# Kernel optimization log

Hardware: AMD Instinct MI355X
Metric: run time of the kernel (lower is better)

Reference implementation:

```python
import jax, jax.numpy as jnp
import numpy as np

KERNEL_D = 3          # cv2 d=3 -> radius 1, 3x3 neighborhood
SIGMA_SPACE = 50.0
SIGMA_COLOR = 2.0
POOL = 16             # downsample_factor


def _bilateral3(x):
    # x: [B, H, W] single-channel images. cv2 BORDER_DEFAULT == REFLECT_101 == jnp 'reflect'.
    B, H, W = x.shape
    xp = jnp.pad(x, ((0, 0), (1, 1), (1, 1)), mode='reflect')
    inv2sc = 1.0 / (2.0 * SIGMA_COLOR * SIGMA_COLOR)
    inv2ss = 1.0 / (2.0 * SIGMA_SPACE * SIGMA_SPACE)
    num = jnp.zeros_like(x)
    den = jnp.zeros_like(x)
    for dy in (-1, 0, 1):
        for dx in (-1, 0, 1):
            nb = xp[:, 1 + dy:H + 1 + dy, 1 + dx:W + 1 + dx]
            ws = np.exp(-(dy * dy + dx * dx) * (1.0 / (2.0 * 50.0 * 50.0))).astype(np.float32)
            w = jnp.exp(-(nb - x) ** 2 * inv2sc) * ws
            num = num + w * nb
            den = den + w
    return num / den


def setup_inputs() -> dict:
    key = jax.random.key(0)
    x = jax.random.normal(key, (16, 1, 1024, 1024), dtype=jnp.float32)
    return {"x": x}


def reference(x):
    B, C, H, W = x.shape  # C == 1
    y = _bilateral3(x[:, 0])                       # [B, H, W]
    y = y[:, None]                                 # [B, 1, H, W]
    # AvgPool2d(16): non-overlapping 16x16 mean
    y = y.reshape(B, 1, H // POOL, POOL, W // POOL, POOL).mean(axis=(3, 5))
    return y
```

## Files before the change

kernel.cpp:

```cpp
#include <hip/hip_runtime.h>

#define IMG_H 1024
#define IMG_W 1024

#define CC  (-0.1803368801111244f)
#define WS1 (-2.8853900817779270e-4f)
#define WS2 (-5.7707801635558540e-4f)

typedef __attribute__((ext_vector_type(2))) float f32x2;

__device__ __forceinline__ float e2(float y) { return __builtin_amdgcn_exp2f(y); }

__device__ __forceinline__ f32x2 earg2(f32x2 u, f32x2 v, float ws) {
    f32x2 d = u - v;
    return __builtin_elementwise_fma(d * d, (f32x2)CC, (f32x2)ws);
}
__device__ __forceinline__ float earg1(float u, float v, float ws) {
    float d = u - v;
    return fmaf(d * d, CC, ws);
}

__global__ __launch_bounds__(256) void EdgePreserve_kernel(const float* __restrict__ x,
                                                           float* __restrict__ out) {
    const int t   = threadIdx.x;
    const int bid = blockIdx.x;
    const int b   = bid >> 6;
    const int pr  = bid & 63;
    const int r0  = pr << 4;
    const int c0  = t << 2;

    const float* base = x + (size_t)b * (IMG_H * IMG_W);
    const int cl = (c0 == 0) ? 1 : c0 - 1;
    const int cr = (c0 + 4 >= IMG_W) ? IMG_W - 2 : c0 + 4;

    float a0,a1,a2,a3,a4,a5, b0,b1,b2,b3,b4,b5, k0,k1,k2,k3,k4,k5, p0,p1,p2,p3,p4,p5;

#define LOADROW(q, d0,d1,d2,d3,d4,d5) { \
    int _r = r0 + (q); \
    int _rr = (_r < 0) ? -_r : ((_r >= IMG_H) ? (2*IMG_H-2-_r) : _r); \
    const float* _rp = base + _rr * IMG_W; \
    float4 _v = *reinterpret_cast<const float4*>(_rp + c0); \
    d0 = _rp[cl]; d1 = _v.x; d2 = _v.y; d3 = _v.z; d4 = _v.w; d5 = _rp[cr]; }

    LOADROW(-1, a0,a1,a2,a3,a4,a5)
    LOADROW( 0, b0,b1,b2,b3,b4,b5)
    LOADROW( 1, k0,k1,k2,k3,k4,k5)
    LOADROW( 2, p0,p1,p2,p3,p4,p5)

    f32x2 cV12, cV34, cDR01, cDR23;
    float pDL2, pDL3, pDL4, pDL5;
    {
        f32x2 aV  = earg2((f32x2){a1,a2}, (f32x2){b1,b2}, WS1);
        f32x2 aVb = earg2((f32x2){a3,a4}, (f32x2){b3,b4}, WS1);
        f32x2 aR  = earg2((f32x2){a0,a1}, (f32x2){b1,b2}, WS2);
        f32x2 aRb = earg2((f32x2){a2,a3}, (f32x2){b3,b4}, WS2);
        f32x2 aL  = earg2((f32x2){a2,a3}, (f32x2){b1,b2}, WS2);
        f32x2 aLb = earg2((f32x2){a4,a5}, (f32x2){b3,b4}, WS2);
        cV12  = (f32x2){e2(aV.x),  e2(aV.y)};
        cV34  = (f32x2){e2(aVb.x), e2(aVb.y)};
        cDR01 = (f32x2){e2(aR.x),  e2(aR.y)};
        cDR23 = (f32x2){e2(aRb.x), e2(aRb.y)};
        pDL2 = e2(aL.x);  pDL3 = e2(aL.y);
        pDL4 = e2(aLb.x); pDL5 = e2(aLb.y);
    }

    f32x2 psum = (f32x2){0.0f, 0.0f};

    #pragma unroll
    for (int r = 0; r < 16; ++r) {
        f32x2 a01={a0,a1}, a12={a1,a2}, a23={a2,a3}, a34={a3,a4}, a45={a4,a5};
        f32x2 b01={b0,b1}, b12={b1,b2}, b23={b2,b3}, b34={b3,b4}, b45={b4,b5};
        f32x2 k01={k0,k1}, k12={k1,k2}, k23={k2,k3}, k34={k3,k4}, k45={k4,k5};

        f32x2 aH01 = earg2(b01, b12, WS1);
        f32x2 aH23 = earg2(b23, b34, WS1);
        float aH4  = earg1(b4, b5, WS1);
        f32x2 aV12 = earg2(b12, k12, WS1);
        f32x2 aV34 = earg2(b34, k34, WS1);
        f32x2 aDL12 = earg2(b12, k01, WS2);
        f32x2 aDL34 = earg2(b34, k23, WS2);
        float aDL5  = earg1(b5, k4, WS2);
        f32x2 aDR01 = earg2(b01, k12, WS2);
        f32x2 aDR23 = earg2(b23, k34, WS2);
        float aDR4  = earg1(b4, k5, WS2);

        float H0 = e2(aH01.x), H1 = e2(aH01.y), H2 = e2(aH23.x), H3 = e2(aH23.y), H4 = e2(aH4);
        float V1 = e2(aV12.x), V2 = e2(aV12.y), V3 = e2(aV34.x), V4 = e2(aV34.y);
        float DL1 = e2(aDL12.x), DL2 = e2(aDL12.y), DL3 = e2(aDL34.x), DL4 = e2(aDL34.y), DL5 = e2(aDL5);
        float DR0 = e2(aDR01.x), DR1 = e2(aDR01.y), DR2 = e2(aDR23.x), DR3 = e2(aDR23.y), DR4 = e2(aDR4);

        f32x2 H01={H0,H1}, H12={H1,H2}, H23={H2,H3}, H34={H3,H4};
        f32x2 V12={V1,V2}, V34={V3,V4};
        f32x2 DL12={DL1,DL2}, DL34={DL3,DL4};
        f32x2 DR01={DR0,DR1}, DR23={DR2,DR3};

#define PIXPAIR(ctr, nAL,nAC,nAR, nBL,nBR, nKL,nKC,nKR, wAL,wAC,wAR, wBL,wBR, wKL,wKC,wKR) { \
        f32x2 num = ctr; \
        num = __builtin_elementwise_fma(wAL, nAL, num); \
        num = __builtin_elementwise_fma(wAC, nAC, num); \
        num = __builtin_elementwise_fma(wAR, nAR, num); \
        num = __builtin_elementwise_fma(wBL, nBL, num); \
        num = __builtin_elementwise_fma(wBR, nBR, num); \
        num = __builtin_elementwise_fma(wKL, nKL, num); \
        num = __builtin_elementwise_fma(wKC, nKC, num); \
        num = __builtin_elementwise_fma(wKR, nKR, num); \
        f32x2 den = ((wAL + wAC) + (wAR + wBL)) + ((wBR + wKL) + (wKC + wKR)); \
        den = den + (f32x2)1.0f; \
        f32x2 rc = (f32x2){__builtin_amdgcn_rcpf(den.x), __builtin_amdgcn_rcpf(den.y)}; \
        psum = __builtin_elementwise_fma(num, rc, psum); }

        PIXPAIR(b12, a01,a12,a23, b01,b23, k01,k12,k23,
                cDR01, cV12, ((f32x2){pDL2,pDL3}), H01, H12, DL12, V12, ((f32x2){DR1,DR2}))
        PIXPAIR(b34, a23,a34,a45, b23,b45, k23,k34,k45,
                cDR23, cV34, ((f32x2){pDL4,pDL5}), H23, H34, DL34, V34, ((f32x2){DR3,DR4}))
#undef PIXPAIR

        a0=b0;a1=b1;a2=b2;a3=b3;a4=b4;a5=b5;
        b0=k0;b1=k1;b2=k2;b3=k3;b4=k4;b5=k5;
        k0=p0;k1=p1;k2=p2;k3=p3;k4=p4;k5=p5;
        cV12 = V12; cV34 = V34; cDR01 = DR01; cDR23 = DR23;
        pDL2 = DL2; pDL3 = DL3; pDL4 = DL4; pDL5 = DL5;
        if (r < 14) { LOADROW(r+3, p0,p1,p2,p3,p4,p5) }
    }
#undef LOADROW

    float ps = psum.x + psum.y;
    ps += __shfl_xor(ps, 1);
    ps += __shfl_xor(ps, 2);

    if ((t & 3) == 0) {
        out[(size_t)bid * 64 + (t >> 2)] = ps * (1.0f / 256.0f);
    }
}

extern "C" void kernel_launch(void* const* d_in, const int* in_sizes, int n_in,
                              void* d_out, int out_size, void* d_ws, size_t ws_size,
                              hipStream_t stream) {
    const float* x = (const float*)d_in[0];
    float* out     = (float*)d_out;
    EdgePreserve_kernel<<<dim3(16 * 64), dim3(256), 0, stream>>>(x, out);
}
```

Measured before the change: 25.07 us.

## Stage input rows through an LDS ring buffer via async global_load_lds

Replaces per-thread direct global loads, including the scalar halo loads at the left and right edges, with asynchronous global-to-LDS copies into an 8-row ring buffer. Each block prefetches several rows ahead, waits with explicit vmcnt counts and a workgroup barrier before every row, and then reads the centre and both neighbour float4s from LDS. The aim is to remove the uncoalesced halo loads and to keep more row loads in flight. In exchange it adds 32 KB of LDS per block, one barrier per row, and a few extra reflected rows fetched past the block's range.

```diff
diff --git a/kernel.cpp b/kernel.cpp
--- a/kernel.cpp
+++ b/kernel.cpp
@@ -8,6 +8,8 @@
 #define WS2 (-5.7707801635558540e-4f)
 
 typedef __attribute__((ext_vector_type(2))) float f32x2;
+typedef __attribute__((address_space(1))) const void gas_t;
+typedef __attribute__((address_space(3))) void las_t;
 
 __device__ __forceinline__ float e2(float y) { return __builtin_amdgcn_exp2f(y); }
 
@@ -20,54 +22,80 @@
     return fmaf(d * d, CC, ws);
 }
 
-__global__ __launch_bounds__(256) void EdgePreserve_kernel(const float* __restrict__ x,
-                                                           float* __restrict__ out) {
-    const int t   = threadIdx.x;
-    const int bid = blockIdx.x;
-    const int b   = bid >> 6;
-    const int pr  = bid & 63;
-    const int r0  = pr << 4;
-    const int c0  = t << 2;
+#define VMCNT(n) asm volatile("s_waitcnt vmcnt(" #n ")" ::: "memory")
+#define BAR()    { asm volatile("" ::: "memory"); __builtin_amdgcn_s_barrier(); asm volatile("" ::: "memory"); }
+
+__global__ __launch_bounds__(256, 4) void EdgePreserve_kernel(const float* __restrict__ x,
+                                                              float* __restrict__ out) {
+    const int t    = threadIdx.x;
+    const int lane = t & 63;
+    const int wid  = t >> 6;
+    const int bid  = blockIdx.x;
+    const int b    = bid >> 6;
+    const int pr   = bid & 63;
+    const int r0   = pr << 4;
+    const int c0   = t << 2;
+
+    __shared__ __align__(16) float lds[8][IMG_W];
 
     const float* base = x + (size_t)b * (IMG_H * IMG_W);
-    const int cl = (c0 == 0) ? 1 : c0 - 1;
-    const int cr = (c0 + 4 >= IMG_W) ? IMG_W - 2 : c0 + 4;
 
-    float a0,a1,a2,a3,a4,a5, b0,b1,b2,b3,b4,b5, k0,k1,k2,k3,k4,k5, p0,p1,p2,p3,p4,p5;
-
-#define LOADROW(q, d0,d1,d2,d3,d4,d5) { \
+#define DMA(q) { \
     int _r = r0 + (q); \
     int _rr = (_r < 0) ? -_r : ((_r >= IMG_H) ? (2*IMG_H-2-_r) : _r); \
-    const float* _rp = base + _rr * IMG_W; \
-    float4 _v = *reinterpret_cast<const float4*>(_rp + c0); \
-    d0 = _rp[cl]; d1 = _v.x; d2 = _v.y; d3 = _v.z; d4 = _v.w; d5 = _rp[cr]; }
+    const float* _src = base + (size_t)_rr * IMG_W + (wid << 8) + (lane << 2); \
+    __builtin_amdgcn_global_load_lds((gas_t*)_src, (las_t*)&lds[((q)+1) & 7][wid << 8], 16, 0, 0); }
 
-    LOADROW(-1, a0,a1,a2,a3,a4,a5)
-    LOADROW( 0, b0,b1,b2,b3,b4,b5)
-    LOADROW( 1, k0,k1,k2,k3,k4,k5)
-    LOADROW( 2, p0,p1,p2,p3,p4,p5)
+    const int cL = (c0 == 0) ? 0 : c0 - 4;
+    const int cR = (c0 == IMG_W - 4) ? IMG_W - 4 : c0 + 4;
+#define READROW(q, d0,d1,d2,d3,d4,d5) { \
+    const int _s = ((q)+1) & 7; \
+    float4 _L = *reinterpret_cast<const float4*>(&lds[_s][cL]); \
+    float4 _C = *reinterpret_cast<const float4*>(&lds[_s][c0]); \
+    float4 _R = *reinterpret_cast<const float4*>(&lds[_s][cR]); \
+    d0 = (c0 == 0) ? _L.y : _L.w; \
+    d1 = _C.x; d2 = _C.y; d3 = _C.z; d4 = _C.w; \
+    d5 = (c0 == IMG_W - 4) ? _R.z : _R.x; }
 
-    f32x2 cV12, cV34, cDR01, cDR23;
-    float pDL2, pDL3, pDL4, pDL5;
-    {
-        f32x2 aV  = earg2((f32x2){a1,a2}, (f32x2){b1,b2}, WS1);
-        f32x2 aVb = earg2((f32x2){a3,a4}, (f32x2){b3,b4}, WS1);
-        f32x2 aR  = earg2((f32x2){a0,a1}, (f32x2){b1,b2}, WS2);
-        f32x2 aRb = earg2((f32x2){a2,a3}, (f32x2){b3,b4}, WS2);
-        f32x2 aL  = earg2((f32x2){a2,a3}, (f32x2){b1,b2}, WS2);
-        f32x2 aLb = earg2((f32x2){a4,a5}, (f32x2){b3,b4}, WS2);
-        cV12  = (f32x2){e2(aV.x),  e2(aV.y)};
-        cV34  = (f32x2){e2(aVb.x), e2(aVb.y)};
-        cDR01 = (f32x2){e2(aR.x),  e2(aR.y)};
-        cDR23 = (f32x2){e2(aRb.x), e2(aRb.y)};
-        pDL2 = e2(aL.x);  pDL3 = e2(aL.y);
-        pDL4 = e2(aLb.x); pDL5 = e2(aLb.y);
-    }
+    DMA(-1) DMA(0) DMA(1) DMA(2) DMA(3)
+    VMCNT(2);
+    BAR();
+
+    float a0,a1,a2,a3,a4,a5, b0,b1,b2,b3,b4,b5, k0,k1,k2,k3,k4,k5;
+    READROW(-1, a0,a1,a2,a3,a4,a5)
+    READROW( 0, b0,b1,b2,b3,b4,b5)
+
+    f32x2 cV12  = (f32x2){e2(earg1(a1,b1,WS1)), e2(earg1(a2,b2,WS1))};
+    f32x2 cV34  = (f32x2){e2(earg1(a3,b3,WS1)), e2(earg1(a4,b4,WS1))};
+    f32x2 cDR01 = (f32x2){e2(earg1(a0,b1,WS2)), e2(earg1(a1,b2,WS2))};
+    f32x2 cDR23 = (f32x2){e2(earg1(a2,b3,WS2)), e2(earg1(a3,b4,WS2))};
+    f32x2 cDL23 = (f32x2){e2(earg1(a2,b1,WS2)), e2(earg1(a3,b2,WS2))};
+    f32x2 cDL45 = (f32x2){e2(earg1(a4,b3,WS2)), e2(earg1(a5,b4,WS2))};
 
     f32x2 psum = (f32x2){0.0f, 0.0f};
 
+#define PIXPAIR(ctr, nAL,nAC,nAR, nBL,nBR, nKL,nKC,nKR, wAL,wAC,wAR, wBL,wBR, wKL,wKC,wKR) { \
+        f32x2 num = ctr; \
+        num = __builtin_elementwise_fma(wAL, nAL, num); \
+        num = __builtin_elementwise_fma(wAC, nAC, num); \
+        num = __builtin_elementwise_fma(wAR, nAR, num); \
+        num = __builtin_elementwise_fma(wBL, nBL, num); \
+        num = __builtin_elementwise_fma(wBR, nBR, num); \
+        num = __builtin_elementwise_fma(wKL, nKL, num); \
+        num = __builtin_elementwise_fma(wKC, nKC, num); \
+        num = __builtin_elementwise_fma(wKR, nKR, num); \
+        f32x2 den = ((wAL + wAC) + (wAR + wBL)) + ((wBR + wKL) + (wKC + wKR)); \
+        den = den + (f32x2)1.0f; \
+        f32x2 rc = (f32x2){__builtin_amdgcn_rcpf(den.x), __builtin_amdgcn_rcpf(den.y)}; \
+        psum = __builtin_elementwise_fma(num, rc, psum); }
+
     #pragma unroll
     for (int r = 0; r < 16; ++r) {
+        DMA(r + 4)
+        VMCNT(3);
+        BAR();
+        READROW(r + 1, k0,k1,k2,k3,k4,k5)
+
         f32x2 a01={a0,a1}, a12={a1,a2}, a23={a2,a3}, a34={a3,a4}, a45={a4,a5};
         f32x2 b01={b0,b1}, b12={b1,b2}, b23={b2,b3}, b34={b3,b4}, b45={b4,b5};
         f32x2 k01={k0,k1}, k12={k1,k2}, k23={k2,k3}, k34={k3,k4}, k45={k4,k5};
@@ -94,35 +122,22 @@
         f32x2 DL12={DL1,DL2}, DL34={DL3,DL4};
         f32x2 DR01={DR0,DR1}, DR23={DR2,DR3};
 
-#define PIXPAIR(ctr, nAL,nAC,nAR, nBL,nBR, nKL,nKC,nKR, wAL,wAC,wAR, wBL,wBR, wKL,wKC,wKR) { \
-        f32x2 num = ctr; \
-        num = __builtin_elementwise_fma(wAL, nAL, num); \
-        num = __builtin_elementwise_fma(wAC, nAC, num); \
-        num = __builtin_elementwise_fma(wAR, nAR, num); \
-        num = __builtin_elementwise_fma(wBL, nBL, num); \
-        num = __builtin_elementwise_fma(wBR, nBR, num); \
-        num = __builtin_elementwise_fma(wKL, nKL, num); \
-        num = __builtin_elementwise_fma(wKC, nKC, num); \
-        num = __builtin_elementwise_fma(wKR, nKR, num); \
-        f32x2 den = ((wAL + wAC) + (wAR + wBL)) + ((wBR + wKL) + (wKC + wKR)); \
-        den = den + (f32x2)1.0f; \
-        f32x2 rc = (f32x2){__builtin_amdgcn_rcpf(den.x), __builtin_amdgcn_rcpf(den.y)}; \
-        psum = __builtin_elementwise_fma(num, rc, psum); }
-
         PIXPAIR(b12, a01,a12,a23, b01,b23, k01,k12,k23,
-                cDR01, cV12, ((f32x2){pDL2,pDL3}), H01, H12, DL12, V12, ((f32x2){DR1,DR2}))
+                cDR01, cV12, cDL23,
+                H01, H12, DL12, V12, ((f32x2){DR1,DR2}))
         PIXPAIR(b34, a23,a34,a45, b23,b45, k23,k34,k45,
-                cDR23, cV34, ((f32x2){pDL4,pDL5}), H23, H34, DL34, V34, ((f32x2){DR3,DR4}))
-#undef PIXPAIR
+                cDR23, cV34, cDL45,
+                H23, H34, DL34, V34, ((f32x2){DR3,DR4}))
 
         a0=b0;a1=b1;a2=b2;a3=b3;a4=b4;a5=b5;
         b0=k0;b1=k1;b2=k2;b3=k3;b4=k4;b5=k5;
-        k0=p0;k1=p1;k2=p2;k3=p3;k4=p4;k5=p5;
         cV12 = V12; cV34 = V34; cDR01 = DR01; cDR23 = DR23;
-        pDL2 = DL2; pDL3 = DL3; pDL4 = DL4; pDL5 = DL5;
-        if (r < 14) { LOADROW(r+3, p0,p1,p2,p3,p4,p5) }
+        cDL23 = (f32x2){DL2, DL3};
+        cDL45 = (f32x2){DL4, DL5};
     }
-#undef LOADROW
+#undef PIXPAIR
+#undef READROW
+#undef DMA
 
     float ps = psum.x + psum.y;
     ps += __shfl_xor(ps, 1);
```

New measurement: 27.88 us. 1.11x slower.
